# Performance work log

Hardware: AMD Instinct MI355X
Metric: run time of the kernel (lower is better)

## Reference

```python
import jax, jax.numpy as jnp
import numpy as np

B = 2048        # graphs per batch
NC = 81         # cells per sudoku
IN_C, HID = 10, 128
N_ACT, N_NUM, N_TECH = 4, 9, 10


def _sudoku_edges():
    idx = np.arange(NC).reshape(9, 9)
    adj = np.zeros((NC, NC), dtype=bool)
    for i in range(9):
        for j in range(9):
            n = idx[i, j]
            adj[n, idx[i, :]] = True
            adj[n, idx[:, j]] = True
            bi, bj = 3 * (i // 3), 3 * (j // 3)
            adj[n, idx[bi:bi + 3, bj:bj + 3].reshape(-1)] = True
            adj[n, n] = False
    src, dst = np.nonzero(adj)  # 1620 directed edges
    return np.stack([src, dst]).astype(np.int32)


def setup_inputs() -> dict:
    key = jax.random.key(0)
    ks = jax.random.split(key, 12)
    N = B * NC
    base = _sudoku_edges()                          # [2, 1620]
    offs = (np.arange(B, dtype=np.int32) * NC)      # [B]
    ei = (base[:, None, :] + offs[None, :, None]).reshape(2, -1)  # [2, B*1620]
    batch = np.repeat(np.arange(B, dtype=np.int32), NC)           # [N]

    def lin(k, fan_in, fan_out):
        s = 1.0 / np.sqrt(fan_in)
        return jax.random.uniform(k, (fan_in, fan_out), jnp.float32, -s, s)

    return {
        "x": jax.random.normal(ks[0], (N, IN_C), jnp.float32),
        "edge_index": jnp.asarray(ei),
        "batch": jnp.asarray(batch),
        "W1": lin(ks[1], IN_C, HID), "b1": jnp.zeros((HID,), jnp.float32),
        "W2": lin(ks[2], HID, HID),  "b2": jnp.zeros((HID,), jnp.float32),
        "Wa": lin(ks[3], HID, N_ACT),  "ba": jnp.zeros((N_ACT,), jnp.float32),
        "Wc": lin(ks[4], HID, NC),     "bc": jnp.zeros((NC,), jnp.float32),
        "Wn": lin(ks[5], HID, N_NUM),  "bn": jnp.zeros((N_NUM,), jnp.float32),
        "Wt": lin(ks[6], HID, N_TECH), "bt": jnp.zeros((N_TECH,), jnp.float32),
    }


def _gcn_conv(x, edge_index, W, b):
    n = x.shape[0]
    loop = jnp.arange(n, dtype=edge_index.dtype)
    src = jnp.concatenate([edge_index[0], loop])
    dst = jnp.concatenate([edge_index[1], loop])
    deg = jax.ops.segment_sum(jnp.ones_like(dst, jnp.float32), dst, num_segments=n)
    dinv = jax.lax.rsqrt(deg)            # deg >= 1 due to self-loops
    norm = dinv[src] * dinv[dst]         # [E+N]
    h = x @ W                            # [N, out]
    msg = h[src] * norm[:, None]         # gather + scale
    return jax.ops.segment_sum(msg, dst, num_segments=n) + b


def reference(x, edge_index, batch, W1, b1, W2, b2, Wa, ba, Wc, bc, Wn, bn, Wt, bt):
    h = jax.nn.relu(_gcn_conv(x, edge_index, W1, b1))
    h = jax.nn.relu(_gcn_conv(h, edge_index, W2, b2))
    # global mean pool over graphs
    sums = jax.ops.segment_sum(h, batch, num_segments=B)
    cnts = jax.ops.segment_sum(jnp.ones((h.shape[0],), h.dtype), batch, num_segments=B)
    pooled = sums / jnp.maximum(cnts, 1.0)[:, None]   # [B, HID]
    return (pooled @ Wa + ba, pooled @ Wc + bc, pooled @ Wn + bn, pooled @ Wt + bt)
```

## Files before the change

### kernel.cpp

```cpp
#include <hip/hip_runtime.h>
#include <hip/hip_bf16.h>

typedef __attribute__((ext_vector_type(8))) short bf16x8;
typedef __attribute__((ext_vector_type(4))) float f32x4;

__device__ __forceinline__ unsigned short f2b(float f) {
    __hip_bfloat16 h = __float2bfloat16(f);
    return __builtin_bit_cast(unsigned short, h);
}
__device__ __forceinline__ float b2f(unsigned short u) {
    unsigned v = ((unsigned)u) << 16;
    return __builtin_bit_cast(float, v);
}
__device__ __forceinline__ float ldf(const void* p, int idx, bool f32) {
    return f32 ? ((const float*)p)[idx] : b2f(((const unsigned short*)p)[idx]);
}
__device__ __forceinline__ unsigned short ldb(const void* p, int idx, bool f32) {
    return f32 ? f2b(((const float*)p)[idx]) : ((const unsigned short*)p)[idx];
}
__device__ __forceinline__ int swz(int row, int col) {
    return row * 128 + (((col >> 3) ^ (row & 7)) << 3) + (col & 7);
}
__device__ __forceinline__ uint2 pk4(f32x4 c) {
    unsigned lo = (unsigned)f2b(c[0]) | ((unsigned)f2b(c[1]) << 16);
    unsigned hi = (unsigned)f2b(c[2]) | ((unsigned)f2b(c[3]) << 16);
    return make_uint2(lo, hi);
}
__device__ __forceinline__ bf16x8 mkB(uint2 a, uint2 b) {
    return __builtin_bit_cast(bf16x8, make_uint4(a.x, a.y, b.x, b.y));
}

__device__ __forceinline__ bool sniff_f32(const void* x) {
    const unsigned* p = (const unsigned*)x;
    int wild = 0;
#pragma unroll
    for (int i = 0; i < 16; ++i) {
        unsigned e = (p[i] >> 7) & 0xFF;
        wild += (e != 0 && (e < 0x68 || e > 0x90)) ? 1 : 0;
    }
    return wild > 8;
}

#define WS_B1F    16
#define WS_B2F    528
#define WS_BHF    1040
#define WS_W1R    1536
#define WS_W2R    9728
#define WS_SR     42496
#define WS_WH     60928

__global__ void k_repack(const void* __restrict__ x,
                         const void* __restrict__ W1, const void* __restrict__ b1,
                         const void* __restrict__ W2, const void* __restrict__ b2,
                         const void* __restrict__ Wa, const void* __restrict__ ba,
                         const void* __restrict__ Wc, const void* __restrict__ bc,
                         const void* __restrict__ Wn, const void* __restrict__ bn,
                         const void* __restrict__ Wt, const void* __restrict__ bt,
                         char* __restrict__ ws) {
    const bool f32 = sniff_f32(x);
    int idx = blockIdx.x * blockDim.x + threadIdx.x;
    if (idx < 4096) {
        int f = idx >> 5, k = idx & 31;
        unsigned short v = (k < 10) ? ldb(W1, k * 128 + f, f32) : (unsigned short)0;
        ((unsigned short*)(ws + WS_W1R))[idx] = v;
        return;
    }
    idx -= 4096;
    if (idx < 16384) {
        int f = idx >> 7, k = idx & 127;
        ((unsigned short*)(ws + WS_W2R))[idx] = ldb(W2, k * 128 + f, f32);
        return;
    }
    idx -= 16384;
    if (idx < 9216) {
        int fi = idx >> 9, rem = idx & 511;
        int lane = rem >> 3, j = rem & 7;
        int mt = fi / 3, s = fi - mt * 3;
        int node = mt * 16 + (lane & 15);
        int qa = lane >> 4;
        int cell = (2 * s + (j >> 2)) * 16 + qa * 4 + (j & 3);
        bool adj = false;
        if (node < 81 && cell < 81) {
            int ni = node / 9, nj = node % 9;
            int ci = cell / 9, cj = cell % 9;
            adj = (ni == ci) || (nj == cj) ||
                  ((ni / 3 == ci / 3) && (nj / 3 == cj / 3));
        }
        ((unsigned short*)(ws + WS_SR))[idx] = adj ? (unsigned short)0x3F80 : (unsigned short)0;
        return;
    }
    idx -= 9216;
    if (idx < 13312) {
        int o = idx >> 7, f = idx & 127;
        const void* W; int oo, dim;
        if (o < 4)       { W = Wa; oo = o;      dim = 4;  }
        else if (o < 85) { W = Wc; oo = o - 4;  dim = 81; }
        else if (o < 94) { W = Wn; oo = o - 85; dim = 9;  }
        else             { W = Wt; oo = o - 94; dim = 10; }
        ((float*)(ws + WS_WH))[idx] = ldf(W, f * dim + oo, f32);
        return;
    }
    idx -= 13312;
    if (idx < 360) {
        float v;
        if (idx < 128)      v = ldf(b1, idx, f32);
        else if (idx < 256) v = ldf(b2, idx - 128, f32);
        else {
            int o = idx - 256;
            if (o < 4)       v = ldf(ba, o, f32);
            else if (o < 85) v = ldf(bc, o - 4, f32);
            else if (o < 94) v = ldf(bn, o - 85, f32);
            else             v = ldf(bt, o - 94, f32);
        }
        if (idx < 128)      ((float*)(ws + WS_B1F))[idx] = v;
        else if (idx < 256) ((float*)(ws + WS_B2F))[idx - 128] = v;
        else                ((float*)(ws + WS_BHF))[idx - 256] = v;
    }
}

__global__ __launch_bounds__(256, 2) void sudoku_gnn(
    const void* __restrict__ x, const char* __restrict__ ws,
    void* __restrict__ out, int nB)
{
    __shared__ __attribute__((aligned(16))) unsigned short hS[2][12288];
    __shared__ __attribute__((aligned(16))) unsigned short sS[9216];
    __shared__ float sPool[2][128];

    const bool f32 = sniff_f32(x);
    const unsigned short* w1r = (const unsigned short*)(ws + WS_W1R);
    const unsigned short* w2r = (const unsigned short*)(ws + WS_W2R);
    const float* b1f = (const float*)(ws + WS_B1F);
    const float* b2f = (const float*)(ws + WS_B2F);
    const float* bhf = (const float*)(ws + WS_BHF);
    const float* whf = (const float*)(ws + WS_WH);

    const int tid  = threadIdx.x;
    const int wave = tid >> 6;
    const int lane = tid & 63;
    const int ln15 = lane & 15;
    const int q    = lane >> 4;
    const int k0   = q * 8;
    const int FB   = wave * 32;
    const int g0   = blockIdx.x * 2;
    const bool hasB = (g0 + 1 < nB);
    const float inv21 = 1.0f / 21.0f;
    const float inv81 = 1.0f / 81.0f;

    uint4 xr4[2][6]; unsigned xr1[2][6];
    if (!f32) {
#pragma unroll
        for (int gg = 0; gg < 2; ++gg) {
            int g = g0 + gg; if (g >= nB) g = nB - 1;
            const char* xg = (const char*)x + (size_t)g * 1620;
#pragma unroll
            for (int mt = 0; mt < 6; ++mt) {
                int node = mt * 16 + ln15;
                uint4 r = {0, 0, 0, 0}; unsigned r1v = 0;
                if (node < 81) {
                    if (q == 0)      r   = *(const uint4*)(xg + node * 20);
                    else if (q == 1) r1v = *(const unsigned*)(xg + node * 20 + 16);
                }
                xr4[gg][mt] = r; xr1[gg][mt] = r1v;
            }
        }
    }

    {
        const uint4* src = (const uint4*)(ws + WS_SR);
        uint4* dst = (uint4*)sS;
        for (int i = tid; i < 1152; i += 256) dst[i] = src[i];
    }

    bf16x8 w1f[2];
#pragma unroll
    for (int fmt = 0; fmt < 2; ++fmt)
        w1f[fmt] = *(const bf16x8*)&w1r[(FB + fmt * 16 + ln15) * 32 + k0];

    const f32x4 z4 = {0.f, 0.f, 0.f, 0.f};

    uint2 tpk[2][6][2];
#pragma unroll
    for (int gg = 0; gg < 2; ++gg)
#pragma unroll
        for (int mt = 0; mt < 6; ++mt) {
            bf16x8 xv = {0, 0, 0, 0, 0, 0, 0, 0};
            if (!f32) {
                if (q == 0)      xv = __builtin_bit_cast(bf16x8, xr4[gg][mt]);
                else if (q == 1) { xv[0] = (short)(xr1[gg][mt] & 0xFFFF); xv[1] = (short)(xr1[gg][mt] >> 16); }
            } else {
                int node = mt * 16 + ln15;
                if (node < 81) {
                    int g = g0 + gg; if (g >= nB) g = nB - 1;
                    const float* xg = (const float*)x + (size_t)g * 810 + node * 10;
                    if (q == 0) {
#pragma unroll
                        for (int j = 0; j < 8; ++j) xv[j] = (short)f2b(xg[j]);
                    } else if (q == 1) {
                        xv[0] = (short)f2b(xg[8]);
                        xv[1] = (short)f2b(xg[9]);
                    }
                }
            }
#pragma unroll
            for (int fmt = 0; fmt < 2; ++fmt)
                tpk[gg][mt][fmt] = pk4(__builtin_amdgcn_mfma_f32_16x16x32_bf16(xv, w1f[fmt], z4, 0, 0, 0));
        }
    __syncthreads();

    f32x4 acc[2][6][2];

#pragma unroll
    for (int a = 0; a < 2; ++a)
#pragma unroll
        for (int b = 0; b < 6; ++b)
#pragma unroll
            for (int c = 0; c < 2; ++c) acc[a][b][c] = z4;
#pragma unroll
    for (int s = 0; s < 3; ++s) {
        bf16x8 B[2][2];
#pragma unroll
        for (int gg = 0; gg < 2; ++gg)
#pragma unroll
            for (int fmt = 0; fmt < 2; ++fmt)
                B[gg][fmt] = mkB(tpk[gg][2 * s][fmt], tpk[gg][2 * s + 1][fmt]);
#pragma unroll
        for (int mt = 0; mt < 6; ++mt) {
            bf16x8 afr = *(const bf16x8*)&sS[((mt * 3 + s) * 64 + lane) * 8];
#pragma unroll
            for (int gg = 0; gg < 2; ++gg)
#pragma unroll
                for (int fmt = 0; fmt < 2; ++fmt)
                    acc[gg][mt][fmt] = __builtin_amdgcn_mfma_f32_16x16x32_bf16(afr, B[gg][fmt], acc[gg][mt][fmt], 0, 0, 0);
        }
    }
#pragma unroll
    for (int gg = 0; gg < 2; ++gg)
#pragma unroll
        for (int fmt = 0; fmt < 2; ++fmt) {
            float bias = b1f[FB + fmt * 16 + ln15];
#pragma unroll
            for (int mt = 0; mt < 6; ++mt)
#pragma unroll
                for (int r = 0; r < 4; ++r) {
                    int cell = mt * 16 + q * 4 + r;
                    float v = fmaxf(acc[gg][mt][fmt][r] * inv21 + bias, 0.0f);
                    hS[gg][swz(cell, FB + fmt * 16 + ln15)] = f2b(v);
                }
        }
    __syncthreads();

#pragma unroll
    for (int a = 0; a < 2; ++a)
#pragma unroll
        for (int b = 0; b < 6; ++b)
#pragma unroll
            for (int c = 0; c < 2; ++c) acc[a][b][c] = z4;
#pragma unroll
    for (int kc = 0; kc < 4; ++kc) {
        bf16x8 w2f[2];
#pragma unroll
        for (int fmt = 0; fmt < 2; ++fmt)
            w2f[fmt] = *(const bf16x8*)&w2r[(FB + fmt * 16 + ln15) * 128 + kc * 32 + k0];
#pragma unroll
        for (int mt = 0; mt < 6; ++mt) {
            bf16x8 a0 = *(const bf16x8*)&hS[0][swz(mt * 16 + ln15, kc * 32 + k0)];
            bf16x8 a1 = *(const bf16x8*)&hS[1][swz(mt * 16 + ln15, kc * 32 + k0)];
#pragma unroll
            for (int fmt = 0; fmt < 2; ++fmt) {
                acc[0][mt][fmt] = __builtin_amdgcn_mfma_f32_16x16x32_bf16(a0, w2f[fmt], acc[0][mt][fmt], 0, 0, 0);
                acc[1][mt][fmt] = __builtin_amdgcn_mfma_f32_16x16x32_bf16(a1, w2f[fmt], acc[1][mt][fmt], 0, 0, 0);
            }
        }
    }
#pragma unroll
    for (int gg = 0; gg < 2; ++gg)
#pragma unroll
        for (int mt = 0; mt < 6; ++mt)
#pragma unroll
            for (int fmt = 0; fmt < 2; ++fmt)
                tpk[gg][mt][fmt] = pk4(acc[gg][mt][fmt]);

#pragma unroll
    for (int a = 0; a < 2; ++a)
#pragma unroll
        for (int b = 0; b < 6; ++b)
#pragma unroll
            for (int c = 0; c < 2; ++c) acc[a][b][c] = z4;
#pragma unroll
    for (int s = 0; s < 3; ++s) {
        bf16x8 B[2][2];
#pragma unroll
        for (int gg = 0; gg < 2; ++gg)
#pragma unroll
            for (int fmt = 0; fmt < 2; ++fmt)
                B[gg][fmt] = mkB(tpk[gg][2 * s][fmt], tpk[gg][2 * s + 1][fmt]);
#pragma unroll
        for (int mt = 0; mt < 6; ++mt) {
            bf16x8 afr = *(const bf16x8*)&sS[((mt * 3 + s) * 64 + lane) * 8];
#pragma unroll
            for (int gg = 0; gg < 2; ++gg)
#pragma unroll
                for (int fmt = 0; fmt < 2; ++fmt)
                    acc[gg][mt][fmt] = __builtin_amdgcn_mfma_f32_16x16x32_bf16(afr, B[gg][fmt], acc[gg][mt][fmt], 0, 0, 0);
        }
    }
#pragma unroll
    for (int gg = 0; gg < 2; ++gg)
#pragma unroll
        for (int fmt = 0; fmt < 2; ++fmt) {
            float bias = b2f[FB + fmt * 16 + ln15];
            float sum = 0.f;
#pragma unroll
            for (int mt = 0; mt < 6; ++mt)
#pragma unroll
                for (int r = 0; r < 4; ++r) {
                    int cell = mt * 16 + q * 4 + r;
                    float v = fmaxf(acc[gg][mt][fmt][r] * inv21 + bias, 0.0f);
                    sum += (cell < 81) ? v : 0.0f;
                }
            sum += __shfl_xor(sum, 16);
            sum += __shfl_xor(sum, 32);
            if (lane < 16) sPool[gg][FB + fmt * 16 + lane] = sum * inv81;
        }
    __syncthreads();

    if (tid < 208) {
        int gg = (tid >= 104) ? 1 : 0;
        int o  = tid - gg * 104;
        int g  = g0 + gg;
        if (gg == 0 || hasB) {
            float a = bhf[o];
            const float4* wrow = (const float4*)(whf + o * 128);
            const float4* sp4  = (const float4*)sPool[gg];
#pragma unroll 8
            for (int i = 0; i < 32; ++i) {
                float4 wv = wrow[i];
                float4 pv = sp4[i];
                a += pv.x * wv.x + pv.y * wv.y + pv.z * wv.z + pv.w * wv.w;
            }
            int oo; size_t off;
            if (o < 4)       { oo = o;      off = (size_t)g * 4 + oo; }
            else if (o < 85) { oo = o - 4;  off = (size_t)nB * 4  + (size_t)g * 81 + oo; }
            else if (o < 94) { oo = o - 85; off = (size_t)nB * 85 + (size_t)g * 9  + oo; }
            else             { oo = o - 94; off = (size_t)nB * 94 + (size_t)g * 10 + oo; }
            if (f32) ((float*)out)[off] = a;
            else     ((unsigned short*)out)[off] = f2b(a);
        }
    }
}

extern "C" void kernel_launch(void* const* d_in, const int* in_sizes, int n_in,
                              void* d_out, int out_size, void* d_ws, size_t ws_size,
                              hipStream_t stream) {
    const void* x  = d_in[0];
    int nB = in_sizes[2] / 81;
    if (nB <= 0) return;

    char* ws = (char*)d_ws;
    hipLaunchKernelGGL(k_repack, dim3(170), dim3(256), 0, stream,
                       x, d_in[3], d_in[4], d_in[5], d_in[6],
                       d_in[7], d_in[8], d_in[9], d_in[10],
                       d_in[11], d_in[12], d_in[13], d_in[14], ws);
    hipLaunchKernelGGL(sudoku_gnn, dim3((nB + 1) / 2), dim3(256), 0, stream,
                       x, (const char*)ws, d_out, nB);
}
```

Measured before the change: 140.3 us.

## Split each block's two graphs across separate wave groups with 512 threads

Each block now uses 512 threads. Waves 0-3 handle the first graph and waves 4-7 the second, where previously each wave looped over both graphs. This halves per-thread accumulator and register state and gives more waves to hide latency, at the cost of larger blocks and duplicated adjacency and weight fragment loads per wave group. The launch bound is now 512 threads with 4 blocks per CU as the occupancy hint.

```diff
diff --git a/kernel.cpp b/kernel.cpp
--- a/kernel.cpp
+++ b/kernel.cpp
@@ -118,7 +118,7 @@
     }
 }
 
-__global__ __launch_bounds__(256, 2) void sudoku_gnn(
+__global__ __launch_bounds__(512, 4) void sudoku_gnn(
     const void* __restrict__ x, const char* __restrict__ ws,
     void* __restrict__ out, int nB)
 {
@@ -136,39 +136,37 @@
 
     const int tid  = threadIdx.x;
     const int wave = tid >> 6;
+    const int gq   = wave >> 2;
     const int lane = tid & 63;
     const int ln15 = lane & 15;
     const int q    = lane >> 4;
     const int k0   = q * 8;
-    const int FB   = wave * 32;
+    const int FB   = (wave & 3) * 32;
     const int g0   = blockIdx.x * 2;
     const bool hasB = (g0 + 1 < nB);
+    const int g    = (g0 + gq < nB) ? g0 + gq : nB - 1;
     const float inv21 = 1.0f / 21.0f;
     const float inv81 = 1.0f / 81.0f;
 
-    uint4 xr4[2][6]; unsigned xr1[2][6];
+    uint4 xr4[6]; unsigned xr1[6];
     if (!f32) {
-#pragma unroll
-        for (int gg = 0; gg < 2; ++gg) {
-            int g = g0 + gg; if (g >= nB) g = nB - 1;
-            const char* xg = (const char*)x + (size_t)g * 1620;
-#pragma unroll
-            for (int mt = 0; mt < 6; ++mt) {
-                int node = mt * 16 + ln15;
-                uint4 r = {0, 0, 0, 0}; unsigned r1v = 0;
-                if (node < 81) {
-                    if (q == 0)      r   = *(const uint4*)(xg + node * 20);
-                    else if (q == 1) r1v = *(const unsigned*)(xg + node * 20 + 16);
-                }
-                xr4[gg][mt] = r; xr1[gg][mt] = r1v;
-            }
+        const char* xg = (const char*)x + (size_t)g * 1620;
+#pragma unroll
+        for (int mt = 0; mt < 6; ++mt) {
+            int node = mt * 16 + ln15;
+            uint4 r = {0, 0, 0, 0}; unsigned r1v = 0;
+            if (node < 81) {
+                if (q == 0)      r   = *(const uint4*)(xg + node * 20);
+                else if (q == 1) r1v = *(const unsigned*)(xg + node * 20 + 16);
+            }
+            xr4[mt] = r; xr1[mt] = r1v;
         }
     }
 
     {
         const uint4* src = (const uint4*)(ws + WS_SR);
         uint4* dst = (uint4*)sS;
-        for (int i = tid; i < 1152; i += 256) dst[i] = src[i];
+        for (int i = tid; i < 1152; i += 512) dst[i] = src[i];
     }
 
     bf16x8 w1f[2];
@@ -178,83 +176,70 @@
 
     const f32x4 z4 = {0.f, 0.f, 0.f, 0.f};
 
-    uint2 tpk[2][6][2];
-#pragma unroll
-    for (int gg = 0; gg < 2; ++gg)
-#pragma unroll
-        for (int mt = 0; mt < 6; ++mt) {
-            bf16x8 xv = {0, 0, 0, 0, 0, 0, 0, 0};
-            if (!f32) {
-                if (q == 0)      xv = __builtin_bit_cast(bf16x8, xr4[gg][mt]);
-                else if (q == 1) { xv[0] = (short)(xr1[gg][mt] & 0xFFFF); xv[1] = (short)(xr1[gg][mt] >> 16); }
-            } else {
-                int node = mt * 16 + ln15;
-                if (node < 81) {
-                    int g = g0 + gg; if (g >= nB) g = nB - 1;
-                    const float* xg = (const float*)x + (size_t)g * 810 + node * 10;
-                    if (q == 0) {
-#pragma unroll
-                        for (int j = 0; j < 8; ++j) xv[j] = (short)f2b(xg[j]);
-                    } else if (q == 1) {
-                        xv[0] = (short)f2b(xg[8]);
-                        xv[1] = (short)f2b(xg[9]);
-                    }
+    uint2 tpk[6][2];
+#pragma unroll
+    for (int mt = 0; mt < 6; ++mt) {
+        bf16x8 xv = {0, 0, 0, 0, 0, 0, 0, 0};
+        if (!f32) {
+            if (q == 0)      xv = __builtin_bit_cast(bf16x8, xr4[mt]);
+            else if (q == 1) { xv[0] = (short)(xr1[mt] & 0xFFFF); xv[1] = (short)(xr1[mt] >> 16); }
+        } else {
+            int node = mt * 16 + ln15;
+            if (node < 81) {
+                const float* xg = (const float*)x + (size_t)g * 810 + node * 10;
+                if (q == 0) {
+#pragma unroll
+                    for (int j = 0; j < 8; ++j) xv[j] = (short)f2b(xg[j]);
+                } else if (q == 1) {
+                    xv[0] = (short)f2b(xg[8]);
+                    xv[1] = (short)f2b(xg[9]);
                 }
             }
-#pragma unroll
-            for (int fmt = 0; fmt < 2; ++fmt)
-                tpk[gg][mt][fmt] = pk4(__builtin_amdgcn_mfma_f32_16x16x32_bf16(xv, w1f[fmt], z4, 0, 0, 0));
-        }
+        }
+#pragma unroll
+        for (int fmt = 0; fmt < 2; ++fmt)
+            tpk[mt][fmt] = pk4(__builtin_amdgcn_mfma_f32_16x16x32_bf16(xv, w1f[fmt], z4, 0, 0, 0));
+    }
     __syncthreads();
 
-    f32x4 acc[2][6][2];
-
-#pragma unroll
-    for (int a = 0; a < 2; ++a)
-#pragma unroll
-        for (int b = 0; b < 6; ++b)
-#pragma unroll
-            for (int c = 0; c < 2; ++c) acc[a][b][c] = z4;
+    f32x4 acc[6][2];
+
+#pragma unroll
+    for (int a = 0; a < 6; ++a)
+#pragma unroll
+        for (int c = 0; c < 2; ++c) acc[a][c] = z4;
 #pragma unroll
     for (int s = 0; s < 3; ++s) {
-        bf16x8 B[2][2];
-#pragma unroll
-        for (int gg = 0; gg < 2; ++gg)
-#pragma unroll
-            for (int fmt = 0; fmt < 2; ++fmt)
-                B[gg][fmt] = mkB(tpk[gg][2 * s][fmt], tpk[gg][2 * s + 1][fmt]);
+        bf16x8 B[2];
+#pragma unroll
+        for (int fmt = 0; fmt < 2; ++fmt)
+            B[fmt] = mkB(tpk[2 * s][fmt], tpk[2 * s + 1][fmt]);
 #pragma unroll
         for (int mt = 0; mt < 6; ++mt) {
             bf16x8 afr = *(const bf16x8*)&sS[((mt * 3 + s) * 64 + lane) * 8];
 #pragma unroll
-            for (int gg = 0; gg < 2; ++gg)
-#pragma unroll
-                for (int fmt = 0; fmt < 2; ++fmt)
-                    acc[gg][mt][fmt] = __builtin_amdgcn_mfma_f32_16x16x32_bf16(afr, B[gg][fmt], acc[gg][mt][fmt], 0, 0, 0);
-        }
-    }
-#pragma unroll
-    for (int gg = 0; gg < 2; ++gg)
-#pragma unroll
-        for (int fmt = 0; fmt < 2; ++fmt) {
-            float bias = b1f[FB + fmt * 16 + ln15];
-#pragma unroll
-            for (int mt = 0; mt < 6; ++mt)
-#pragma unroll
-                for (int r = 0; r < 4; ++r) {
-                    int cell = mt * 16 + q * 4 + r;
-                    float v = fmaxf(acc[gg][mt][fmt][r] * inv21 + bias, 0.0f);
-                    hS[gg][swz(cell, FB + fmt * 16 + ln15)] = f2b(v);
-                }
-        }
+            for (int fmt = 0; fmt < 2; ++fmt)
+                acc[mt][fmt] = __builtin_amdgcn_mfma_f32_16x16x32_bf16(afr, B[fmt], acc[mt][fmt], 0, 0, 0);
+        }
+    }
+#pragma unroll
+    for (int fmt = 0; fmt < 2; ++fmt) {
+        float bias = b1f[FB + fmt * 16 + ln15];
+#pragma unroll
+        for (int mt = 0; mt < 6; ++mt)
+#pragma unroll
+            for (int r = 0; r < 4; ++r) {
+                int cell = mt * 16 + q * 4 + r;
+                float v = fmaxf(acc[mt][fmt][r] * inv21 + bias, 0.0f);
+                hS[gq][swz(cell, FB + fmt * 16 + ln15)] = f2b(v);
+            }
+    }
     __syncthreads();
 
 #pragma unroll
-    for (int a = 0; a < 2; ++a)
-#pragma unroll
-        for (int b = 0; b < 6; ++b)
-#pragma unroll
-            for (int c = 0; c < 2; ++c) acc[a][b][c] = z4;
+    for (int a = 0; a < 6; ++a)
+#pragma unroll
+        for (int c = 0; c < 2; ++c) acc[a][c] = z4;
 #pragma unroll
     for (int kc = 0; kc < 4; ++kc) {
         bf16x8 w2f[2];
@@ -263,71 +248,58 @@
             w2f[fmt] = *(const bf16x8*)&w2r[(FB + fmt * 16 + ln15) * 128 + kc * 32 + k0];
 #pragma unroll
         for (int mt = 0; mt < 6; ++mt) {
-            bf16x8 a0 = *(const bf16x8*)&hS[0][swz(mt * 16 + ln15, kc * 32 + k0)];
-            bf16x8 a1 = *(const bf16x8*)&hS[1][swz(mt * 16 + ln15, kc * 32 + k0)];
-#pragma unroll
-            for (int fmt = 0; fmt < 2; ++fmt) {
-                acc[0][mt][fmt] = __builtin_amdgcn_mfma_f32_16x16x32_bf16(a0, w2f[fmt], acc[0][mt][fmt], 0, 0, 0);
-                acc[1][mt][fmt] = __builtin_amdgcn_mfma_f32_16x16x32_bf16(a1, w2f[fmt], acc[1][mt][fmt], 0, 0, 0);
-            }
-        }
-    }
-#pragma unroll
-    for (int gg = 0; gg < 2; ++gg)
-#pragma unroll
-        for (int mt = 0; mt < 6; ++mt)
+            bf16x8 a3 = *(const bf16x8*)&hS[gq][swz(mt * 16 + ln15, kc * 32 + k0)];
 #pragma unroll
             for (int fmt = 0; fmt < 2; ++fmt)
-                tpk[gg][mt][fmt] = pk4(acc[gg][mt][fmt]);
-
-#pragma unroll
-    for (int a = 0; a < 2; ++a)
-#pragma unroll
-        for (int b = 0; b < 6; ++b)
-#pragma unroll
-            for (int c = 0; c < 2; ++c) acc[a][b][c] = z4;
+                acc[mt][fmt] = __builtin_amdgcn_mfma_f32_16x16x32_bf16(a3, w2f[fmt], acc[mt][fmt], 0, 0, 0);
+        }
+    }
+#pragma unroll
+    for (int mt = 0; mt < 6; ++mt)
+#pragma unroll
+        for (int fmt = 0; fmt < 2; ++fmt)
+            tpk[mt][fmt] = pk4(acc[mt][fmt]);
+
+#pragma unroll
+    for (int a = 0; a < 6; ++a)
+#pragma unroll
+        for (int c = 0; c < 2; ++c) acc[a][c] = z4;
 #pragma unroll
     for (int s = 0; s < 3; ++s) {
-        bf16x8 B[2][2];
-#pragma unroll
-        for (int gg = 0; gg < 2; ++gg)
-#pragma unroll
-            for (int fmt = 0; fmt < 2; ++fmt)
-                B[gg][fmt] = mkB(tpk[gg][2 * s][fmt], tpk[gg][2 * s + 1][fmt]);
+        bf16x8 B[2];
+#pragma unroll
+        for (int fmt = 0; fmt < 2; ++fmt)
+            B[fmt] = mkB(tpk[2 * s][fmt], tpk[2 * s + 1][fmt]);
 #pragma unroll
         for (int mt = 0; mt < 6; ++mt) {
             bf16x8 afr = *(const bf16x8*)&sS[((mt * 3 + s) * 64 + lane) * 8];
 #pragma unroll
-            for (int gg = 0; gg < 2; ++gg)
-#pragma unroll
-                for (int fmt = 0; fmt < 2; ++fmt)
-                    acc[gg][mt][fmt] = __builtin_amdgcn_mfma_f32_16x16x32_bf16(afr, B[gg][fmt], acc[gg][mt][fmt], 0, 0, 0);
-        }
-    }
-#pragma unroll
-    for (int gg = 0; gg < 2; ++gg)
-#pragma unroll
-        for (int fmt = 0; fmt < 2; ++fmt) {
-            float bias = b2f[FB + fmt * 16 + ln15];
-            float sum = 0.f;
-#pragma unroll
-            for (int mt = 0; mt < 6; ++mt)
-#pragma unroll
-                for (int r = 0; r < 4; ++r) {
-                    int cell = mt * 16 + q * 4 + r;
-                    float v = fmaxf(acc[gg][mt][fmt][r] * inv21 + bias, 0.0f);
-                    sum += (cell < 81) ? v : 0.0f;
-                }
-            sum += __shfl_xor(sum, 16);
-            sum += __shfl_xor(sum, 32);
-            if (lane < 16) sPool[gg][FB + fmt * 16 + lane] = sum * inv81;
-        }
+            for (int fmt = 0; fmt < 2; ++fmt)
+                acc[mt][fmt] = __builtin_amdgcn_mfma_f32_16x16x32_bf16(afr, B[fmt], acc[mt][fmt], 0, 0, 0);
+        }
+    }
+#pragma unroll
+    for (int fmt = 0; fmt < 2; ++fmt) {
+        float bias = b2f[FB + fmt * 16 + ln15];
+        float sum = 0.f;
+#pragma unroll
+        for (int mt = 0; mt < 6; ++mt)
+#pragma unroll
+            for (int r = 0; r < 4; ++r) {
+                int cell = mt * 16 + q * 4 + r;
+                float v = fmaxf(acc[mt][fmt][r] * inv21 + bias, 0.0f);
+                sum += (cell < 81) ? v : 0.0f;
+            }
+        sum += __shfl_xor(sum, 16);
+        sum += __shfl_xor(sum, 32);
+        if (lane < 16) sPool[gq][FB + fmt * 16 + lane] = sum * inv81;
+    }
     __syncthreads();
 
     if (tid < 208) {
         int gg = (tid >= 104) ? 1 : 0;
         int o  = tid - gg * 104;
-        int g  = g0 + gg;
+        int gh = g0 + gg;
         if (gg == 0 || hasB) {
             float a = bhf[o];
             const float4* wrow = (const float4*)(whf + o * 128);
@@ -339,10 +311,10 @@
                 a += pv.x * wv.x + pv.y * wv.y + pv.z * wv.z + pv.w * wv.w;
             }
             int oo; size_t off;
-            if (o < 4)       { oo = o;      off = (size_t)g * 4 + oo; }
-            else if (o < 85) { oo = o - 4;  off = (size_t)nB * 4  + (size_t)g * 81 + oo; }
-            else if (o < 94) { oo = o - 85; off = (size_t)nB * 85 + (size_t)g * 9  + oo; }
-            else             { oo = o - 94; off = (size_t)nB * 94 + (size_t)g * 10 + oo; }
+            if (o < 4)       { oo = o;      off = (size_t)gh * 4 + oo; }
+            else if (o < 85) { oo = o - 4;  off = (size_t)nB * 4  + (size_t)gh * 81 + oo; }
+            else if (o < 94) { oo = o - 85; off = (size_t)nB * 85 + (size_t)gh * 9  + oo; }
+            else             { oo = o - 94; off = (size_t)nB * 94 + (size_t)gh * 10 + oo; }
             if (f32) ((float*)out)[off] = a;
             else     ((unsigned short*)out)[off] = f2b(a);
         }
@@ -361,6 +333,6 @@
                        x, d_in[3], d_in[4], d_in[5], d_in[6],
                        d_in[7], d_in[8], d_in[9], d_in[10],
                        d_in[11], d_in[12], d_in[13], d_in[14], ws);
-    hipLaunchKernelGGL(sudoku_gnn, dim3((nB + 1) / 2), dim3(256), 0, stream,
+    hipLaunchKernelGGL(sudoku_gnn, dim3((nB + 1) / 2), dim3(512), 0, stream,
                        x, (const char*)ws, d_out, nB);
 }
```

After: 136.7 us. -2.6%, faster.
